# Kernel optimization log

Measured on AMD Instinct MI355X. Metric: run time of the kernel, lower is better.

The kernel has to match this reference:

```python
import jax, jax.numpy as jnp
import numpy as np

DEPTH, HEADS, DIM_HEAD = 3, 8, 64
DIM = 512
MAX_SEQ = 2048
INNER = HEADS * DIM_HEAD  # 512
FF_HID = 4 * DIM          # 2048
EPS = 1e-5


def sparsemax(z):
    # z: (..., n); sparsemax projection onto the simplex (Martins & Astudillo 2016)
    n = z.shape[-1]
    z_sorted = jnp.flip(jnp.sort(z, axis=-1), axis=-1)            # descending
    cs = jnp.cumsum(z_sorted, axis=-1)
    ks = jnp.arange(1, n + 1, dtype=z.dtype)
    support = 1.0 + ks * z_sorted > cs                            # bool
    k_z = jnp.sum(support, axis=-1, keepdims=True)                # int support size
    cs_k = jnp.take_along_axis(cs, k_z - 1, axis=-1)
    tau = (cs_k - 1.0) / k_z.astype(z.dtype)
    return jnp.maximum(z - tau, 0.0)


def layernorm(x, g, b):
    mu = jnp.mean(x, axis=-1, keepdims=True)
    var = jnp.mean(jnp.square(x - mu), axis=-1, keepdims=True)
    return (x - mu) * jax.lax.rsqrt(var + EPS) * g + b


def setup_inputs() -> dict:
    key = jax.random.key(0)
    ks = jax.random.split(key, 12)
    s = 0.02
    inp = {
        "x": jax.random.normal(ks[0], (8, 1024, DIM), dtype=jnp.float32),
        "proj_w": jax.random.normal(ks[1], (DIM, DIM), dtype=jnp.float32) * s,
        "proj_b": jnp.zeros((DIM,), dtype=jnp.float32),
        "pos_emb": jax.random.normal(ks[2], (MAX_SEQ, DIM), dtype=jnp.float32) * s,
        "ln1_g": jnp.ones((DEPTH, DIM), dtype=jnp.float32),
        "ln1_b": jnp.zeros((DEPTH, DIM), dtype=jnp.float32),
        "wqkv": jax.random.normal(ks[3], (DEPTH, DIM, 3 * INNER), dtype=jnp.float32) * s,
        "wout": jax.random.normal(ks[4], (DEPTH, INNER, DIM), dtype=jnp.float32) * s,
        "bout": jnp.zeros((DEPTH, DIM), dtype=jnp.float32),
        "ln2_g": jnp.ones((DEPTH, DIM), dtype=jnp.float32),
        "ln2_b": jnp.zeros((DEPTH, DIM), dtype=jnp.float32),
        "w1": jax.random.normal(ks[5], (DEPTH, DIM, 2 * FF_HID), dtype=jnp.float32) * s,
        "b1": jnp.zeros((DEPTH, 2 * FF_HID), dtype=jnp.float32),
        "w2": jax.random.normal(ks[6], (DEPTH, FF_HID, DIM), dtype=jnp.float32) * s,
        "b2": jnp.zeros((DEPTH, DIM), dtype=jnp.float32),
    }
    return inp


def reference(x, proj_w, proj_b, pos_emb, ln1_g, ln1_b, wqkv, wout, bout,
              ln2_g, ln2_b, w1, b1, w2, b2):
    B, S, D = x.shape
    scale = DIM_HEAD ** -0.5
    x = x @ proj_w + proj_b                       # projection
    x = x + pos_emb[:S][None, :, :]               # positional embedding
    for l in range(DEPTH):
        # --- attention block (Residual(PreNorm(Attention))) ---
        h = layernorm(x, ln1_g[l], ln1_b[l])
        qkv = h @ wqkv[l]                         # (B,S,3*INNER)
        q, k, v = jnp.split(qkv, 3, axis=-1)
        rs = lambda t: t.reshape(B, S, HEADS, DIM_HEAD).transpose(0, 2, 1, 3)
        q, k, v = rs(q), rs(k), rs(v)             # (B,H,S,Dh)
        sim = jnp.einsum('bhid,bhjd->bhij', q, k) * scale
        attn = sparsemax(sim)
        out = jnp.einsum('bhij,bhjd->bhid', attn, v)
        out = out.transpose(0, 2, 1, 3).reshape(B, S, INNER)
        x = x + (out @ wout[l] + bout[l])
        # --- feedforward block (Residual(PreNorm(GEGLU FFN))) ---
        h = layernorm(x, ln2_g[l], ln2_b[l])
        hh = h @ w1[l] + b1[l]                    # (B,S,2*FF_HID)
        a, g = jnp.split(hh, 2, axis=-1)
        ff = (a * jax.nn.gelu(g, approximate=False)) @ w2[l] + b2[l]
        x = x + ff
    return jnp.mean(x, axis=1)                    # (B, D) mean pool
```

## Files before the change

### kernel.cpp

```cpp
#include <hip/hip_runtime.h>
#include <stdint.h>

typedef unsigned short u16;
typedef __attribute__((ext_vector_type(8))) short short8;
typedef __attribute__((ext_vector_type(4))) float f32x4;

__device__ __forceinline__ float bf2f(u16 u){
  union { unsigned u; float f; } v; v.u = ((unsigned)u) << 16; return v.f;
}
__device__ __forceinline__ u16 f2bf(float f){
  union { float f; unsigned u; } v; v.f = f;
  unsigned u = v.u;
  return (u16)((u + 0x7FFFu + ((u >> 16) & 1u)) >> 16);
}
__device__ __forceinline__ void g2lds16(const u16* g, u16* lds){
  __builtin_amdgcn_global_load_lds(
      (const __attribute__((address_space(1))) unsigned int*)g,
      (__attribute__((address_space(3))) unsigned int*)lds, 16, 0, 0);
}
__device__ __forceinline__ float gelu_fast(float g){
  float u2 = g * (1.5957691216057308f + 0.0713548162726f * g * g);
  return g * __builtin_amdgcn_rcpf(1.0f + __expf(-u2));
}

__global__ void k_flag(const unsigned* __restrict__ ln1g, int* __restrict__ flag){
  if (threadIdx.x == 0 && blockIdx.x == 0)
    *flag = (ln1g[0] == 0x3F800000u) ? 0 : 1;
}

__global__ void k_cvt_f32(const void* __restrict__ src, float* __restrict__ dst, int n,
                          const int* __restrict__ flag){
  int i = blockIdx.x * blockDim.x + threadIdx.x;
  if (i < n) dst[i] = (*flag) ? bf2f(((const u16*)src)[i]) : ((const float*)src)[i];
}
__global__ void k_cvt_bf16(const void* __restrict__ src, u16* __restrict__ dst, int n,
                           const int* __restrict__ flag){
  int i = blockIdx.x * blockDim.x + threadIdx.x;
  if (i < n) dst[i] = (*flag) ? ((const u16*)src)[i] : f2bf(((const float*)src)[i]);
}

__global__ void k_transpose(const void* __restrict__ src, u16* __restrict__ dst,
                            int K, int N, const int* __restrict__ flag){
  __shared__ u16 tile[32][33];
  int n0 = blockIdx.x * 32, k0 = blockIdx.y * 32;
  size_t zsrc = (size_t)blockIdx.z * K * N;
  size_t zdst = (size_t)blockIdx.z * N * K;
  int tx = threadIdx.x & 31, ty = threadIdx.x >> 5;
  bool isbf = (*flag) != 0;
  const float* sf = (const float*)src; const u16* sb = (const u16*)src;
  #pragma unroll
  for (int p = 0; p < 4; ++p){
    int kk = k0 + p*8 + ty, nn = n0 + tx;
    size_t idx = zsrc + (size_t)kk * N + nn;
    tile[tx][p*8+ty] = isbf ? sb[idx] : f2bf(sf[idx]);
  }
  __syncthreads();
  #pragma unroll
  for (int p = 0; p < 4; ++p){
    int nn = n0 + p*8 + ty, kk = k0 + tx;
    dst[zdst + (size_t)nn * K + kk] = tile[p*8+ty][tx];
  }
}

__global__ __launch_bounds__(256) void k_ln(const float* __restrict__ x,
                                            const float* __restrict__ g,
                                            const float* __restrict__ b,
                                            u16* __restrict__ out){
  int wv = threadIdx.x >> 6, lane = threadIdx.x & 63;
  int row = blockIdx.x * 4 + wv;
  const float* xr = x + (size_t)row * 512 + lane * 8;
  float4 v0 = *(const float4*)xr;
  float4 v1 = *(const float4*)(xr + 4);
  float s  = v0.x+v0.y+v0.z+v0.w + v1.x+v1.y+v1.z+v1.w;
  float ss = v0.x*v0.x+v0.y*v0.y+v0.z*v0.z+v0.w*v0.w
           + v1.x*v1.x+v1.y*v1.y+v1.z*v1.z+v1.w*v1.w;
  #pragma unroll
  for (int off = 1; off < 64; off <<= 1){ s += __shfl_xor(s, off, 64); ss += __shfl_xor(ss, off, 64); }
  float mu = s * (1.f/512.f);
  float var = ss * (1.f/512.f) - mu*mu;
  float rs = rsqrtf(var + 1e-5f);
  const float* gp = g + lane*8; const float* bp = b + lane*8;
  float4 g0 = *(const float4*)gp, g1 = *(const float4*)(gp+4);
  float4 b0 = *(const float4*)bp, b1 = *(const float4*)(bp+4);
  u16 o[8];
  o[0]=f2bf((v0.x-mu)*rs*g0.x+b0.x); o[1]=f2bf((v0.y-mu)*rs*g0.y+b0.y);
  o[2]=f2bf((v0.z-mu)*rs*g0.z+b0.z); o[3]=f2bf((v0.w-mu)*rs*g0.w+b0.w);
  o[4]=f2bf((v1.x-mu)*rs*g1.x+b1.x); o[5]=f2bf((v1.y-mu)*rs*g1.y+b1.y);
  o[6]=f2bf((v1.z-mu)*rs*g1.z+b1.z); o[7]=f2bf((v1.w-mu)*rs*g1.w+b1.w);
  *(uint4*)(out + (size_t)row*512 + lane*8) = *(const uint4*)o;
}

__global__ __launch_bounds__(256) void k_gemm(const u16* __restrict__ A,
                                              const u16* __restrict__ Wt, int K, int mode,
                                              float* __restrict__ xres, u16* __restrict__ out16,
                                              const float* __restrict__ bias,
                                              const float* __restrict__ pos){
  __shared__ u16 As[128*64];
  __shared__ u16 Bs[128*64];
  const int tid = threadIdx.x;
  const int wv = tid >> 6, lane = tid & 63;
  const int lm = lane & 15, lq = lane >> 4;
  const int wm = (wv >> 1) * 64, wn = (wv & 1) * 64;
  const int m0 = blockIdx.y * 128, n0 = blockIdx.x * 128;
  const int lrow = lane >> 3;
  const int scol = ((lane & 7) ^ lrow) << 3;
  f32x4 acc[4][4];
  #pragma unroll
  for (int i = 0; i < 4; ++i)
    #pragma unroll
    for (int j = 0; j < 4; ++j){ f32x4 z = {0.f,0.f,0.f,0.f}; acc[i][j] = z; }

  for (int k0 = 0; k0 < K; k0 += 64){
    #pragma unroll
    for (int it = 0; it < 4; ++it){
      int ci = wv*4 + it;
      int row = ci*8 + lrow;
      g2lds16(&A [(size_t)(m0 + row) * K + k0 + scol], &As[ci*512]);
      g2lds16(&Wt[(size_t)(n0 + row) * K + k0 + scol], &Bs[ci*512]);
    }
    __syncthreads();
    #pragma unroll
    for (int kk = 0; kk < 2; ++kk){
      short8 af[4], bf[4];
      #pragma unroll
      for (int t = 0; t < 4; ++t){
        int cs = ((kk*4 + lq) ^ (lm & 7)) << 3;
        af[t] = *(const short8*)&As[(wm + t*16 + lm)*64 + cs];
        bf[t] = *(const short8*)&Bs[(wn + t*16 + lm)*64 + cs];
      }
      #pragma unroll
      for (int i = 0; i < 4; ++i)
        #pragma unroll
        for (int j = 0; j < 4; ++j)
          acc[i][j] = __builtin_amdgcn_mfma_f32_16x16x32_bf16(af[i], bf[j], acc[i][j], 0, 0, 0);
    }
    __syncthreads();
  }
  #pragma unroll
  for (int i = 0; i < 4; ++i)
    #pragma unroll
    for (int j = 0; j < 4; ++j)
      #pragma unroll
      for (int r = 0; r < 4; ++r){
        int row = m0 + wm + i*16 + lq*4 + r;
        int col = n0 + wn + j*16 + lm;
        float v = acc[i][j][r];
        if (mode == 0){
          xres[(size_t)row*512 + col] = v + bias[col] + pos[(size_t)(row & 1023)*512 + col];
        } else if (mode == 1){
          int part = col >> 9, within = col & 511;
          int head = within >> 6, dh = within & 63;
          int b = row >> 10, s = row & 1023;
          int bh = b*8 + head;
          size_t o;
          if (part < 2) o = (size_t)part*4194304 + (((size_t)bh*1024 + s) << 6) + dh;
          else          o = (size_t)8388608 + (size_t)bh*65536 + (size_t)dh*1024 + s;
          out16[o] = f2bf(v);
        } else {
          size_t idx = (size_t)row*512 + col;
          xres[idx] = xres[idx] + v + bias[col];
        }
      }
}

__global__ __launch_bounds__(256) void k_gemm64(const u16* __restrict__ A,
                                                const u16* __restrict__ Wt, int K, int mode,
                                                float* __restrict__ xres,
                                                const float* __restrict__ bias,
                                                const float* __restrict__ pos){
  __shared__ u16 As[64*64];
  __shared__ u16 Bs[128*64];
  const int tid = threadIdx.x;
  const int wv = tid >> 6, lane = tid & 63;
  const int lm = lane & 15, lq = lane >> 4;
  const int wm = (wv >> 1) * 32, wn = (wv & 1) * 64;
  const int m0 = blockIdx.y * 64, n0 = blockIdx.x * 128;
  const int lrow = lane >> 3;
  const int scol = ((lane & 7) ^ lrow) << 3;
  f32x4 acc[2][4];
  #pragma unroll
  for (int i = 0; i < 2; ++i)
    #pragma unroll
    for (int j = 0; j < 4; ++j){ f32x4 z = {0.f,0.f,0.f,0.f}; acc[i][j] = z; }

  for (int k0 = 0; k0 < K; k0 += 64){
    #pragma unroll
    for (int it = 0; it < 2; ++it){
      int ci = wv*2 + it;
      int row = ci*8 + lrow;
      g2lds16(&A[(size_t)(m0 + row) * K + k0 + scol], &As[ci*512]);
    }
    #pragma unroll
    for (int it = 0; it < 4; ++it){
      int ci = wv*4 + it;
      int row = ci*8 + lrow;
      g2lds16(&Wt[(size_t)(n0 + row) * K + k0 + scol], &Bs[ci*512]);
    }
    __syncthreads();
    #pragma unroll
    for (int kk = 0; kk < 2; ++kk){
      short8 af[2], bf[4];
      int cs = ((kk*4 + lq) ^ (lm & 7)) << 3;
      #pragma unroll
      for (int t = 0; t < 2; ++t)
        af[t] = *(const short8*)&As[(wm + t*16 + lm)*64 + cs];
      #pragma unroll
      for (int t = 0; t < 4; ++t)
        bf[t] = *(const short8*)&Bs[(wn + t*16 + lm)*64 + cs];
      #pragma unroll
      for (int i = 0; i < 2; ++i)
        #pragma unroll
        for (int j = 0; j < 4; ++j)
          acc[i][j] = __builtin_amdgcn_mfma_f32_16x16x32_bf16(af[i], bf[j], acc[i][j], 0, 0, 0);
    }
    __syncthreads();
  }
  #pragma unroll
  for (int i = 0; i < 2; ++i)
    #pragma unroll
    for (int j = 0; j < 4; ++j)
      #pragma unroll
      for (int r = 0; r < 4; ++r){
        int row = m0 + wm + i*16 + lq*4 + r;
        int col = n0 + wn + j*16 + lm;
        float v = acc[i][j][r];
        if (mode == 0){
          xres[(size_t)row*512 + col] = v + bias[col] + pos[(size_t)(row & 1023)*512 + col];
        } else {
          size_t idx = (size_t)row*512 + col;
          xres[idx] = xres[idx] + v + bias[col];
        }
      }
}

__global__ __launch_bounds__(256) void k_ff1_geglu64(const u16* __restrict__ A,
                                                     const u16* __restrict__ W1t,
                                                     const float* __restrict__ b1,
                                                     u16* __restrict__ ffh){
  __shared__ u16 As[64*64];
  __shared__ u16 Ba[128*64];
  __shared__ u16 Bg[128*64];
  const int tid = threadIdx.x;
  const int wv = tid >> 6, lane = tid & 63;
  const int lm = lane & 15, lq = lane >> 4;
  const int wm = (wv >> 1) * 32, wn = (wv & 1) * 64;
  const int m0 = blockIdx.y * 64, n0 = blockIdx.x * 128;
  const int lrow = lane >> 3;
  const int scol = ((lane & 7) ^ lrow) << 3;
  const int K = 512;
  f32x4 aa[2][4], ag[2][4];
  #pragma unroll
  for (int i = 0; i < 2; ++i)
    #pragma unroll
    for (int j = 0; j < 4; ++j){ f32x4 z = {0.f,0.f,0.f,0.f}; aa[i][j] = z; ag[i][j] = z; }
  for (int k0 = 0; k0 < K; k0 += 64){
    #pragma unroll
    for (int it = 0; it < 2; ++it){
      int ci = wv*2 + it;
      int row = ci*8 + lrow;
      g2lds16(&A[(size_t)(m0 + row) * K + k0 + scol], &As[ci*512]);
    }
    #pragma unroll
    for (int it = 0; it < 4; ++it){
      int ci = wv*4 + it;
      int row = ci*8 + lrow;
      g2lds16(&W1t[(size_t)(n0 + row) * K + k0 + scol],        &Ba[ci*512]);
      g2lds16(&W1t[(size_t)(2048 + n0 + row) * K + k0 + scol], &Bg[ci*512]);
    }
    __syncthreads();
    #pragma unroll
    for (int kk = 0; kk < 2; ++kk){
      short8 af[2], ba[4], bg[4];
      int cs = ((kk*4 + lq) ^ (lm & 7)) << 3;
      #pragma unroll
      for (int t = 0; t < 2; ++t)
        af[t] = *(const short8*)&As[(wm + t*16 + lm)*64 + cs];
      #pragma unroll
      for (int t = 0; t < 4; ++t){
        ba[t] = *(const short8*)&Ba[(wn + t*16 + lm)*64 + cs];
        bg[t] = *(const short8*)&Bg[(wn + t*16 + lm)*64 + cs];
      }
      #pragma unroll
      for (int i = 0; i < 2; ++i)
        #pragma unroll
        for (int j = 0; j < 4; ++j){
          aa[i][j] = __builtin_amdgcn_mfma_f32_16x16x32_bf16(af[i], ba[j], aa[i][j], 0, 0, 0);
          ag[i][j] = __builtin_amdgcn_mfma_f32_16x16x32_bf16(af[i], bg[j], ag[i][j], 0, 0, 0);
        }
    }
    __syncthreads();
  }
  #pragma unroll
  for (int i = 0; i < 2; ++i)
    #pragma unroll
    for (int j = 0; j < 4; ++j)
      #pragma unroll
      for (int r = 0; r < 4; ++r){
        int row = m0 + wm + i*16 + lq*4 + r;
        int n = n0 + wn + j*16 + lm;
        float a = aa[i][j][r] + b1[n];
        float g = ag[i][j][r] + b1[2048 + n];
        ffh[(size_t)row*2048 + n] = f2bf(a * gelu_fast(g));
      }
}

__global__ __launch_bounds__(256) void k_qk(const u16* __restrict__ qb,
                                            const u16* __restrict__ kb,
                                            u16* __restrict__ S, int bh0){
  __shared__ u16 As[128*64];
  __shared__ u16 Bs[128*64];
  const int tid = threadIdx.x;
  const int wv = tid >> 6, lane = tid & 63;
  const int lm = lane & 15, lq = lane >> 4;
  const int wm = (wv >> 1) * 64, wn = (wv & 1) * 64;
  const int m0 = blockIdx.y * 128, n0 = blockIdx.x * 128;
  const int lrow = lane >> 3;
  const int scol = ((lane & 7) ^ lrow) << 3;
  const size_t base = (size_t)(bh0 + blockIdx.z) * 65536;
  f32x4 acc[4][4];
  #pragma unroll
  for (int i = 0; i < 4; ++i)
    #pragma unroll
    for (int j = 0; j < 4; ++j){ f32x4 z = {0.f,0.f,0.f,0.f}; acc[i][j] = z; }

  #pragma unroll
  for (int it = 0; it < 4; ++it){
    int ci = wv*4 + it;
    int row = ci*8 + lrow;
    g2lds16(&qb[base + (size_t)(m0 + row) * 64 + scol], &As[ci*512]);
    g2lds16(&kb[base + (size_t)(n0 + row) * 64 + scol], &Bs[ci*512]);
  }
  __syncthreads();
  #pragma unroll
  for (int kk = 0; kk < 2; ++kk){
    short8 af[4], bf[4];
    #pragma unroll
    for (int t = 0; t < 4; ++t){
      int cs = ((kk*4 + lq) ^ (lm & 7)) << 3;
      af[t] = *(const short8*)&As[(wm + t*16 + lm)*64 + cs];
      bf[t] = *(const short8*)&Bs[(wn + t*16 + lm)*64 + cs];
    }
    #pragma unroll
    for (int i = 0; i < 4; ++i)
      #pragma unroll
      for (int j = 0; j < 4; ++j)
        acc[i][j] = __builtin_amdgcn_mfma_f32_16x16x32_bf16(af[i], bf[j], acc[i][j], 0, 0, 0);
  }
  size_t sb = (size_t)blockIdx.z * 1048576;
  #pragma unroll
  for (int i = 0; i < 4; ++i)
    #pragma unroll
    for (int j = 0; j < 4; ++j)
      #pragma unroll
      for (int r = 0; r < 4; ++r){
        int row = m0 + wm + i*16 + lq*4 + r;
        int col = n0 + wn + j*16 + lm;
        S[sb + (size_t)row*1024 + col] = f2bf(acc[i][j][r] * 0.125f);
      }
}

__global__ __launch_bounds__(256) void k_spmax(const u16* __restrict__ S,
                                               u16* __restrict__ P){
  const int lane = threadIdx.x & 63;
  const int row = blockIdx.x * 4 + (threadIdx.x >> 6);
  const u16* src = S + (size_t)row * 1024 + lane * 16;
  u16 zb[16];
  *(uint4*)zb       = *(const uint4*)src;
  *(uint4*)(zb + 8) = *(const uint4*)(src + 8);
  float z[16];
  #pragma unroll
  for (int i = 0; i < 16; ++i) z[i] = bf2f(zb[i]);
  float s = 0.f;
  #pragma unroll
  for (int i = 0; i < 16; ++i) s += z[i];
  #pragma unroll
  for (int off = 1; off < 64; off <<= 1) s += __shfl_xor(s, off, 64);
  float tau = (s - 1.0f) * (1.0f/1024.0f);
  int prevc = 1024;
  for (int it = 0; it < 48; ++it){
    float s2 = 0.f; int c = 0;
    #pragma unroll
    for (int i = 0; i < 16; ++i){
      float p = z[i] - tau;
      s2 += (p > 0.f ? p : 0.f);
      c += (int)__popcll(__ballot(z[i] > tau));
    }
    #pragma unroll
    for (int off = 1; off < 64; off <<= 1) s2 += __shfl_xor(s2, off, 64);
    tau += (s2 - 1.0f) / (float)c;
    if (c == prevc) break;
    prevc = c;
  }
  u16 tmp[16];
  #pragma unroll
  for (int i = 0; i < 16; ++i){
    float p = z[i] - tau; p = p > 0.f ? p : 0.f;
    tmp[i] = f2bf(p);
  }
  u16* dst = P + (size_t)row * 1024 + lane * 16;
  *(uint4*)dst       = *(const uint4*)tmp;
  *(uint4*)(dst + 8) = *(const uint4*)(tmp + 8);
}

__global__ __launch_bounds__(256) void k_pv(const u16* __restrict__ P,
                                            const u16* __restrict__ vt,
                                            u16* __restrict__ aout, int bh0){
  __shared__ u16 As[64*64];
  __shared__ u16 Bs[64*64];
  const int tid = threadIdx.x;
  const int wv = tid >> 6, lane = tid & 63;
  const int lm = lane & 15, lq = lane >> 4;
  const int m0 = blockIdx.x * 64;
  const int bh = bh0 + blockIdx.y;
  const size_t pbase = (size_t)blockIdx.y * 1048576;
  const size_t vbase = (size_t)bh * 65536;
  const int lrow = lane >> 3;
  const int scol = ((lane & 7) ^ lrow) << 3;
  f32x4 acc[4];
  #pragma unroll
  for (int j = 0; j < 4; ++j){ f32x4 z = {0.f,0.f,0.f,0.f}; acc[j] = z; }

  for (int k0 = 0; k0 < 1024; k0 += 64){
    #pragma unroll
    for (int it = 0; it < 2; ++it){
      int ci = wv*2 + it;
      int row = ci*8 + lrow;
      g2lds16(&P [pbase + (size_t)(m0 + row) * 1024 + k0 + scol], &As[ci*512]);
      g2lds16(&vt[vbase + (size_t)row * 1024 + k0 + scol],        &Bs[ci*512]);
    }
    __syncthreads();
    #pragma unroll
    for (int kk = 0; kk < 2; ++kk){
      int csa = ((kk*4 + lq) ^ (lm & 7)) << 3;
      short8 af = *(const short8*)&As[(wv*16 + lm)*64 + csa];
      #pragma unroll
      for (int j = 0; j < 4; ++j){
        short8 bf = *(const short8*)&Bs[(j*16 + lm)*64 + csa];
        acc[j] = __builtin_amdgcn_mfma_f32_16x16x32_bf16(af, bf, acc[j], 0, 0, 0);
      }
    }
    __syncthreads();
  }
  int b = bh >> 3, h = bh & 7;
  #pragma unroll
  for (int j = 0; j < 4; ++j)
    #pragma unroll
    for (int r = 0; r < 4; ++r){
      int s = m0 + wv*16 + lq*4 + r;
      int d = j*16 + lm;
      aout[((size_t)(b*1024 + s))*512 + h*64 + d] = f2bf(acc[j][r]);
    }
}

__global__ __launch_bounds__(256) void k_attn(const u16* __restrict__ qb,
                                              const u16* __restrict__ kb,
                                              const u16* __restrict__ vt,
                                              u16* __restrict__ aout){
  extern __shared__ char smem[];
  float* sc = (float*)smem;
  u16*  P   = (u16*)smem;
  u16*  Qs  = (u16*)(smem + 131072);
  u16*  KVs = (u16*)(smem + 131072 + 4608);
  const int tid = threadIdx.x;
  const int wv = tid >> 6, lane = tid & 63;
  const int lm = lane & 15, lq = lane >> 4;
  const int bh = blockIdx.y, s0 = blockIdx.x * 32;
  const size_t base = (size_t)bh * 65536;
  {
    int r = tid >> 3, c = tid & 7;
    *(uint4*)&Qs[r*72 + (c << 3)] = *(const uint4*)&qb[base + (size_t)(s0 + r)*64 + (c << 3)];
  }
  for (int kt = 0; kt < 16; ++kt){
    __syncthreads();
    #pragma unroll
    for (int it = 0; it < 2; ++it){
      int s = it*256 + tid; int r = s >> 3, c = s & 7;
      *(uint4*)&KVs[r*72 + (c << 3)] =
          *(const uint4*)&kb[base + (size_t)(kt*64 + r)*64 + (c << 3)];
    }
    __syncthreads();
    f32x4 accs[2];
    { f32x4 z = {0.f,0.f,0.f,0.f}; accs[0] = z; accs[1] = z; }
    #pragma unroll
    for (int kk = 0; kk < 2; ++kk){
      short8 bfk = *(const short8*)&KVs[(wv*16 + lm)*72 + kk*32 + lq*8];
      #pragma unroll
      for (int mt = 0; mt < 2; ++mt){
        short8 af = *(const short8*)&Qs[(mt*16 + lm)*72 + kk*32 + lq*8];
        accs[mt] = __builtin_amdgcn_mfma_f32_16x16x32_bf16(af, bfk, accs[mt], 0, 0, 0);
      }
    }
    #pragma unroll
    for (int mt = 0; mt < 2; ++mt)
      #pragma unroll
      for (int r = 0; r < 4; ++r){
        int row = mt*16 + lq*4 + r;
        int col = kt*64 + wv*16 + lm;
        sc[row*1024 + (((col >> 2) ^ (row & 7)) << 2) + (col & 3)] = accs[mt][r] * 0.125f;
      }
  }
  __syncthreads();
  for (int rr = 0; rr < 8; ++rr){
    int row = wv*8 + rr;
    float z[16];
    #pragma unroll
    for (int i = 0; i < 16; ++i){
      int col = lane + (i << 6);
      z[i] = sc[row*1024 + (((col >> 2) ^ (row & 7)) << 2) + (col & 3)];
    }
    bool act[16];
    #pragma unroll
    for (int i = 0; i < 16; ++i) act[i] = true;
    float prevc = -1.f, tau = 0.f;
    for (int it = 0; it < 64; ++it){
      float s = 0.f, c = 0.f;
      #pragma unroll
      for (int i = 0; i < 16; ++i) if (act[i]){ s += z[i]; c += 1.f; }
      #pragma unroll
      for (int off = 1; off < 64; off <<= 1){ s += __shfl_xor(s, off, 64); c += __shfl_xor(c, off, 64); }
      tau = (s - 1.0f) / c;
      if (c == prevc) break;
      prevc = c;
      #pragma unroll
      for (int i = 0; i < 16; ++i) act[i] = z[i] > tau;
    }
    #pragma unroll
    for (int i = 0; i < 16; ++i){
      int col = lane + (i << 6);
      float p = z[i] - tau; p = p > 0.f ? p : 0.f;
      P[row*2048 + (((col >> 3) ^ (row & 7)) << 3) + (col & 7)] = f2bf(p);
    }
  }
  f32x4 acco[2];
  { f32x4 z = {0.f,0.f,0.f,0.f}; acco[0] = z; acco[1] = z; }
  for (int kt = 0; kt < 16; ++kt){
    __syncthreads();
    {
      int dc = tid >> 6, key = tid & 63;
      #pragma unroll
      for (int j = 0; j < 16; ++j)
        KVs[(dc*16 + j)*72 + key] = vt[base + (size_t)(dc*16 + j)*1024 + kt*64 + key];
    }
    __syncthreads();
    #pragma unroll
    for (int kk = 0; kk < 2; ++kk){
      short8 bfv = *(const short8*)&KVs[(wv*16 + lm)*72 + kk*32 + lq*8];
      #pragma unroll
      for (int mt = 0; mt < 2; ++mt){
        int m = mt*16 + lm;
        int k = kt*64 + kk*32 + lq*8;
        short8 af = *(const short8*)&P[m*2048 + (((k >> 3) ^ (m & 7)) << 3)];
        acco[mt] = __builtin_amdgcn_mfma_f32_16x16x32_bf16(af, bfv, acco[mt], 0, 0, 0);
      }
    }
  }
  int b = bh >> 3, h = bh & 7;
  #pragma unroll
  for (int mt = 0; mt < 2; ++mt)
    #pragma unroll
    for (int r = 0; r < 4; ++r){
      int row = mt*16 + lq*4 + r;
      int s = s0 + row;
      aout[((size_t)(b*1024 + s))*512 + h*64 + wv*16 + lm] = f2bf(acco[mt][r]);
    }
}

__global__ __launch_bounds__(256) void k_pool1(const float* __restrict__ xres,
                                               float* __restrict__ part){
  int b = blockIdx.y, ch = blockIdx.x, tid = threadIdx.x;
  float a0 = 0.f, a1 = 0.f;
  for (int i = 0; i < 64; ++i){
    const float* r = xres + ((size_t)(b*1024 + ch*64 + i)) * 512;
    a0 += r[tid]; a1 += r[tid + 256];
  }
  part[((size_t)(b*16 + ch))*512 + tid]       = a0;
  part[((size_t)(b*16 + ch))*512 + tid + 256] = a1;
}
__global__ __launch_bounds__(512) void k_pool2(const float* __restrict__ part,
                                               void* __restrict__ out,
                                               const int* __restrict__ flag){
  int b = blockIdx.x, d = threadIdx.x;
  float s = 0.f;
  for (int c = 0; c < 16; ++c) s += part[((size_t)(b*16 + c))*512 + d];
  s *= (1.0f/1024.0f);
  if (*flag) ((u16*)out)[b*512 + d] = f2bf(s);
  else       ((float*)out)[b*512 + d] = s;
}

extern "C" void kernel_launch(void* const* d_in, const int* in_sizes, int n_in,
                              void* d_out, int out_size, void* d_ws, size_t ws_size,
                              hipStream_t stream){
  (void)in_sizes; (void)n_in; (void)out_size;
  char* w = (char*)d_ws;
  size_t off = 0;
  auto alloc = [&](size_t bytes) -> char* {
    char* p = w + off;
    off += (bytes + 255) & ~(size_t)255;
    return p;
  };
  int*   flag  = (int*)  alloc(4);
  float* xres  = (float*)alloc((size_t)8192*512*4);
  u16*   hb    = (u16*)  alloc((size_t)8192*512*2);
  u16*   qb    = (u16*)  alloc((size_t)8388608);
  u16*   kb    = (u16*)  alloc((size_t)8388608);
  u16*   vtb   = (u16*)  alloc((size_t)8388608);
  u16*   aoutb = (u16*)  alloc((size_t)8388608);
  u16*   ffh   = qb;
  u16*   pwT   = (u16*)  alloc((size_t)512*512*2);
  u16*   wqkvT = (u16*)  alloc((size_t)3*1536*512*2);
  u16*   woutT = (u16*)  alloc((size_t)3*512*512*2);
  u16*   w1T   = (u16*)  alloc((size_t)3*4096*512*2);
  u16*   w2T   = (u16*)  alloc((size_t)3*512*2048*2);
  float* posf  = (float*)alloc((size_t)1024*512*4);
  float* pbf   = (float*)alloc(512*4);
  float* ln1gf = (float*)alloc(1536*4);
  float* ln1bf = (float*)alloc(1536*4);
  float* ln2gf = (float*)alloc(1536*4);
  float* ln2bf = (float*)alloc(1536*4);
  float* boutf = (float*)alloc(1536*4);
  float* b1f   = (float*)alloc(12288*4);
  float* b2f   = (float*)alloc(1536*4);
  float* part  = (float*)alloc((size_t)8*16*512*4);

  int chunk = 0;
  u16* Sbuf = nullptr; u16* Pbuf = nullptr;
  {
    size_t rem = (ws_size > off) ? (ws_size - off) : 0;
    for (int c = 64; c >= 8; c >>= 1){
      size_t need = (size_t)c * 1048576 * 4 + 512;
      if (need <= rem){
        Sbuf = (u16*)alloc((size_t)c * 1048576 * 2);
        Pbuf = (u16*)alloc((size_t)c * 1048576 * 2);
        chunk = c;
        break;
      }
    }
  }

  const void* x_raw = d_in[0];  const void* projw = d_in[1];  const void* projb = d_in[2];
  const void* pose  = d_in[3];  const void* ln1g  = d_in[4];  const void* ln1b  = d_in[5];
  const void* wqkv  = d_in[6];  const void* wout  = d_in[7];  const void* bout  = d_in[8];
  const void* ln2g  = d_in[9];  const void* ln2b  = d_in[10]; const void* w1    = d_in[11];
  const void* b1    = d_in[12]; const void* w2    = d_in[13]; const void* b2    = d_in[14];

  k_flag<<<1, 1, 0, stream>>>((const unsigned*)ln1g, flag);

  k_transpose<<<dim3(16, 16, 1), 256, 0, stream>>>(projw, pwT,   512,  512, flag);
  k_transpose<<<dim3(48, 16, 3), 256, 0, stream>>>(wqkv,  wqkvT, 512, 1536, flag);
  k_transpose<<<dim3(16, 16, 3), 256, 0, stream>>>(wout,  woutT, 512,  512, flag);
  k_transpose<<<dim3(128,16, 3), 256, 0, stream>>>(w1,    w1T,   512, 4096, flag);
  k_transpose<<<dim3(16, 64, 3), 256, 0, stream>>>(w2,    w2T,  2048,  512, flag);

  k_cvt_f32<<<2,    256, 0, stream>>>(projb, pbf,    512,    flag);
  k_cvt_f32<<<2048, 256, 0, stream>>>(pose,  posf,   524288, flag);
  k_cvt_f32<<<6,    256, 0, stream>>>(ln1g,  ln1gf,  1536,   flag);
  k_cvt_f32<<<6,    256, 0, stream>>>(ln1b,  ln1bf,  1536,   flag);
  k_cvt_f32<<<6,    256, 0, stream>>>(ln2g,  ln2gf,  1536,   flag);
  k_cvt_f32<<<6,    256, 0, stream>>>(ln2b,  ln2bf,  1536,   flag);
  k_cvt_f32<<<6,    256, 0, stream>>>(bout,  boutf,  1536,   flag);
  k_cvt_f32<<<48,   256, 0, stream>>>(b1,    b1f,    12288,  flag);
  k_cvt_f32<<<6,    256, 0, stream>>>(b2,    b2f,    1536,   flag);
  k_cvt_bf16<<<16384, 256, 0, stream>>>(x_raw, hb, 4194304, flag);

  k_gemm64<<<dim3(4, 128), 256, 0, stream>>>(hb, pwT, 512, 0, xres, pbf, posf);

  for (int l = 0; l < 3; ++l){
    k_ln<<<2048, 256, 0, stream>>>(xres, ln1gf + l*512, ln1bf + l*512, hb);
    k_gemm<<<dim3(12, 64), 256, 0, stream>>>(hb, wqkvT + (size_t)l*1536*512, 512, 1,
                                             nullptr, qb, nullptr, nullptr);
    if (chunk){
      for (int bh0 = 0; bh0 < 64; bh0 += chunk){
        k_qk<<<dim3(8, 8, chunk), 256, 0, stream>>>(qb, kb, Sbuf, bh0);
        k_spmax<<<chunk*256, 256, 0, stream>>>(Sbuf, Pbuf);
        k_pv<<<dim3(16, chunk), 256, 0, stream>>>(Pbuf, vtb, aoutb, bh0);
      }
    } else {
      k_attn<<<dim3(32, 64), 256, 144896, stream>>>(qb, kb, vtb, aoutb);
    }
    k_gemm64<<<dim3(4, 128), 256, 0, stream>>>(aoutb, woutT + (size_t)l*512*512, 512, 2,
                                               xres, boutf + l*512, nullptr);
    k_ln<<<2048, 256, 0, stream>>>(xres, ln2gf + l*512, ln2bf + l*512, hb);
    k_ff1_geglu64<<<dim3(16, 128), 256, 0, stream>>>(hb, w1T + (size_t)l*4096*512,
                                                     b1f + l*4096, ffh);
    k_gemm64<<<dim3(4, 128), 256, 0, stream>>>(ffh, w2T + (size_t)l*512*2048, 2048, 2,
                                               xres, b2f + l*512, nullptr);
  }
  k_pool1<<<dim3(16, 8), 256, 0, stream>>>(xres, part);
  k_pool2<<<8, 512, 0, stream>>>(part, d_out, flag);
}
```

Measured before the change: 1.080 ms.

## Fuse QK, sparsemax and PV into one LDS-resident attention kernel

Replaces the three-kernel attention path (QK scores to global, sparsemax, PV) and the old fallback with a single kernel. Each 256-thread block handles 16 query rows of one head, keeps the 16x1024 bf16 score tile in swizzled LDS, runs sparsemax in place, then does PV straight from LDS. A block-id remap spreads heads across the grid. This removes the large global score and probability round trips and most launches, but each block rereads K and V from global without LDS staging, and the sparsemax iteration now starts from the minimum threshold, which may need more iterations.

```diff
diff --git a/kernel.cpp b/kernel.cpp
--- a/kernel.cpp
+++ b/kernel.cpp
@@ -304,265 +304,90 @@
       }
 }
 
-__global__ __launch_bounds__(256) void k_qk(const u16* __restrict__ qb,
-                                            const u16* __restrict__ kb,
-                                            u16* __restrict__ S, int bh0){
-  __shared__ u16 As[128*64];
-  __shared__ u16 Bs[128*64];
+__global__ __launch_bounds__(256) void k_attn2(const u16* __restrict__ qb,
+                                               const u16* __restrict__ kb,
+                                               const u16* __restrict__ vt,
+                                               u16* __restrict__ aout){
+  __shared__ u16 Sm[16*1024];
   const int tid = threadIdx.x;
   const int wv = tid >> 6, lane = tid & 63;
   const int lm = lane & 15, lq = lane >> 4;
-  const int wm = (wv >> 1) * 64, wn = (wv & 1) * 64;
-  const int m0 = blockIdx.y * 128, n0 = blockIdx.x * 128;
-  const int lrow = lane >> 3;
-  const int scol = ((lane & 7) ^ lrow) << 3;
-  const size_t base = (size_t)(bh0 + blockIdx.z) * 65536;
-  f32x4 acc[4][4];
-  #pragma unroll
-  for (int i = 0; i < 4; ++i)
-    #pragma unroll
-    for (int j = 0; j < 4; ++j){ f32x4 z = {0.f,0.f,0.f,0.f}; acc[i][j] = z; }
-
-  #pragma unroll
-  for (int it = 0; it < 4; ++it){
-    int ci = wv*4 + it;
-    int row = ci*8 + lrow;
-    g2lds16(&qb[base + (size_t)(m0 + row) * 64 + scol], &As[ci*512]);
-    g2lds16(&kb[base + (size_t)(n0 + row) * 64 + scol], &Bs[ci*512]);
+  int fid = blockIdx.x;
+  int nf = (fid & 7) * 512 + (fid >> 3);
+  const int bh = nf >> 6;
+  const int q0 = (nf & 63) * 16;
+  const size_t base = (size_t)bh * 65536;
+  const u16* qp = &qb[base + (size_t)(q0 + lm)*64 + lq*8];
+  short8 qf0 = *(const short8*)qp;
+  short8 qf1 = *(const short8*)(qp + 32);
+  for (int kt = 0; kt < 16; ++kt){
+    const u16* kp = &kb[base + (size_t)(kt*64 + wv*16 + lm)*64 + lq*8];
+    short8 kf0 = *(const short8*)kp;
+    short8 kf1 = *(const short8*)(kp + 32);
+    f32x4 a = {0.f,0.f,0.f,0.f};
+    a = __builtin_amdgcn_mfma_f32_16x16x32_bf16(qf0, kf0, a, 0, 0, 0);
+    a = __builtin_amdgcn_mfma_f32_16x16x32_bf16(qf1, kf1, a, 0, 0, 0);
+    int col = kt*64 + wv*16 + lm;
+    int cc = col >> 3, c7 = col & 7;
+    #pragma unroll
+    for (int r = 0; r < 4; ++r){
+      int row = lq*4 + r;
+      Sm[row*1024 + ((cc ^ (row & 7)) << 3) + c7] = f2bf(a[r] * 0.125f);
+    }
   }
   __syncthreads();
-  #pragma unroll
-  for (int kk = 0; kk < 2; ++kk){
-    short8 af[4], bf[4];
-    #pragma unroll
-    for (int t = 0; t < 4; ++t){
-      int cs = ((kk*4 + lq) ^ (lm & 7)) << 3;
-      af[t] = *(const short8*)&As[(wm + t*16 + lm)*64 + cs];
-      bf[t] = *(const short8*)&Bs[(wn + t*16 + lm)*64 + cs];
-    }
-    #pragma unroll
-    for (int i = 0; i < 4; ++i)
-      #pragma unroll
-      for (int j = 0; j < 4; ++j)
-        acc[i][j] = __builtin_amdgcn_mfma_f32_16x16x32_bf16(af[i], bf[j], acc[i][j], 0, 0, 0);
-  }
-  size_t sb = (size_t)blockIdx.z * 1048576;
-  #pragma unroll
-  for (int i = 0; i < 4; ++i)
-    #pragma unroll
-    for (int j = 0; j < 4; ++j)
-      #pragma unroll
-      for (int r = 0; r < 4; ++r){
-        int row = m0 + wm + i*16 + lq*4 + r;
-        int col = n0 + wn + j*16 + lm;
-        S[sb + (size_t)row*1024 + col] = f2bf(acc[i][j][r] * 0.125f);
-      }
-}
-
-__global__ __launch_bounds__(256) void k_spmax(const u16* __restrict__ S,
-                                               u16* __restrict__ P){
-  const int lane = threadIdx.x & 63;
-  const int row = blockIdx.x * 4 + (threadIdx.x >> 6);
-  const u16* src = S + (size_t)row * 1024 + lane * 16;
-  u16 zb[16];
-  *(uint4*)zb       = *(const uint4*)src;
-  *(uint4*)(zb + 8) = *(const uint4*)(src + 8);
-  float z[16];
-  #pragma unroll
-  for (int i = 0; i < 16; ++i) z[i] = bf2f(zb[i]);
-  float s = 0.f;
-  #pragma unroll
-  for (int i = 0; i < 16; ++i) s += z[i];
-  #pragma unroll
-  for (int off = 1; off < 64; off <<= 1) s += __shfl_xor(s, off, 64);
-  float tau = (s - 1.0f) * (1.0f/1024.0f);
-  int prevc = 1024;
-  for (int it = 0; it < 48; ++it){
-    float s2 = 0.f; int c = 0;
+  #pragma unroll 1
+  for (int rr = 0; rr < 4; ++rr){
+    int row = wv*4 + rr;
+    int r7 = row & 7;
+    u16* lo = &Sm[row*1024 + ((lane ^ r7) << 3)];
+    u16* hi = &Sm[row*1024 + (((64 + lane) ^ r7) << 3)];
+    u16 zb[16];
+    *(uint4*)zb       = *(const uint4*)lo;
+    *(uint4*)(zb + 8) = *(const uint4*)hi;
+    float z[16];
+    #pragma unroll
+    for (int i = 0; i < 16; ++i) z[i] = bf2f(zb[i]);
+    float tau = -3.0e38f;
+    int prevc = -1;
+    for (int it = 0; it < 48; ++it){
+      float sz = 0.f; int c = 0;
+      #pragma unroll
+      for (int i = 0; i < 16; ++i){
+        bool aq = z[i] > tau;
+        sz += aq ? z[i] : 0.f;
+        c  += (int)__popcll(__ballot(aq));
+      }
+      #pragma unroll
+      for (int off = 1; off < 64; off <<= 1) sz += __shfl_xor(sz, off, 64);
+      tau = (sz - 1.0f) / (float)c;
+      if (c == prevc) break;
+      prevc = c;
+    }
+    u16 pb[16];
     #pragma unroll
     for (int i = 0; i < 16; ++i){
       float p = z[i] - tau;
-      s2 += (p > 0.f ? p : 0.f);
-      c += (int)__popcll(__ballot(z[i] > tau));
-    }
-    #pragma unroll
-    for (int off = 1; off < 64; off <<= 1) s2 += __shfl_xor(s2, off, 64);
-    tau += (s2 - 1.0f) / (float)c;
-    if (c == prevc) break;
-    prevc = c;
-  }
-  u16 tmp[16];
-  #pragma unroll
-  for (int i = 0; i < 16; ++i){
-    float p = z[i] - tau; p = p > 0.f ? p : 0.f;
-    tmp[i] = f2bf(p);
-  }
-  u16* dst = P + (size_t)row * 1024 + lane * 16;
-  *(uint4*)dst       = *(const uint4*)tmp;
-  *(uint4*)(dst + 8) = *(const uint4*)(tmp + 8);
-}
-
-__global__ __launch_bounds__(256) void k_pv(const u16* __restrict__ P,
-                                            const u16* __restrict__ vt,
-                                            u16* __restrict__ aout, int bh0){
-  __shared__ u16 As[64*64];
-  __shared__ u16 Bs[64*64];
-  const int tid = threadIdx.x;
-  const int wv = tid >> 6, lane = tid & 63;
-  const int lm = lane & 15, lq = lane >> 4;
-  const int m0 = blockIdx.x * 64;
-  const int bh = bh0 + blockIdx.y;
-  const size_t pbase = (size_t)blockIdx.y * 1048576;
-  const size_t vbase = (size_t)bh * 65536;
-  const int lrow = lane >> 3;
-  const int scol = ((lane & 7) ^ lrow) << 3;
-  f32x4 acc[4];
-  #pragma unroll
-  for (int j = 0; j < 4; ++j){ f32x4 z = {0.f,0.f,0.f,0.f}; acc[j] = z; }
-
-  for (int k0 = 0; k0 < 1024; k0 += 64){
-    #pragma unroll
-    for (int it = 0; it < 2; ++it){
-      int ci = wv*2 + it;
-      int row = ci*8 + lrow;
-      g2lds16(&P [pbase + (size_t)(m0 + row) * 1024 + k0 + scol], &As[ci*512]);
-      g2lds16(&vt[vbase + (size_t)row * 1024 + k0 + scol],        &Bs[ci*512]);
-    }
-    __syncthreads();
-    #pragma unroll
-    for (int kk = 0; kk < 2; ++kk){
-      int csa = ((kk*4 + lq) ^ (lm & 7)) << 3;
-      short8 af = *(const short8*)&As[(wv*16 + lm)*64 + csa];
-      #pragma unroll
-      for (int j = 0; j < 4; ++j){
-        short8 bf = *(const short8*)&Bs[(j*16 + lm)*64 + csa];
-        acc[j] = __builtin_amdgcn_mfma_f32_16x16x32_bf16(af, bf, acc[j], 0, 0, 0);
-      }
-    }
-    __syncthreads();
+      pb[i] = f2bf(p > 0.f ? p : 0.f);
+    }
+    *(uint4*)lo = *(const uint4*)pb;
+    *(uint4*)hi = *(const uint4*)(pb + 8);
+  }
+  __syncthreads();
+  f32x4 acc = {0.f,0.f,0.f,0.f};
+  const u16* vrow = &vt[base + (size_t)(wv*16 + lm)*1024 + lq*8];
+  for (int k0 = 0; k0 < 1024; k0 += 32){
+    int cc = (k0 >> 3) + lq;
+    short8 pa = *(const short8*)&Sm[lm*1024 + ((cc ^ (lm & 7)) << 3)];
+    short8 vb = *(const short8*)(vrow + k0);
+    acc = __builtin_amdgcn_mfma_f32_16x16x32_bf16(pa, vb, acc, 0, 0, 0);
   }
   int b = bh >> 3, h = bh & 7;
   #pragma unroll
-  for (int j = 0; j < 4; ++j)
-    #pragma unroll
-    for (int r = 0; r < 4; ++r){
-      int s = m0 + wv*16 + lq*4 + r;
-      int d = j*16 + lm;
-      aout[((size_t)(b*1024 + s))*512 + h*64 + d] = f2bf(acc[j][r]);
-    }
-}
-
-__global__ __launch_bounds__(256) void k_attn(const u16* __restrict__ qb,
-                                              const u16* __restrict__ kb,
-                                              const u16* __restrict__ vt,
-                                              u16* __restrict__ aout){
-  extern __shared__ char smem[];
-  float* sc = (float*)smem;
-  u16*  P   = (u16*)smem;
-  u16*  Qs  = (u16*)(smem + 131072);
-  u16*  KVs = (u16*)(smem + 131072 + 4608);
-  const int tid = threadIdx.x;
-  const int wv = tid >> 6, lane = tid & 63;
-  const int lm = lane & 15, lq = lane >> 4;
-  const int bh = blockIdx.y, s0 = blockIdx.x * 32;
-  const size_t base = (size_t)bh * 65536;
-  {
-    int r = tid >> 3, c = tid & 7;
-    *(uint4*)&Qs[r*72 + (c << 3)] = *(const uint4*)&qb[base + (size_t)(s0 + r)*64 + (c << 3)];
-  }
-  for (int kt = 0; kt < 16; ++kt){
-    __syncthreads();
-    #pragma unroll
-    for (int it = 0; it < 2; ++it){
-      int s = it*256 + tid; int r = s >> 3, c = s & 7;
-      *(uint4*)&KVs[r*72 + (c << 3)] =
-          *(const uint4*)&kb[base + (size_t)(kt*64 + r)*64 + (c << 3)];
-    }
-    __syncthreads();
-    f32x4 accs[2];
-    { f32x4 z = {0.f,0.f,0.f,0.f}; accs[0] = z; accs[1] = z; }
-    #pragma unroll
-    for (int kk = 0; kk < 2; ++kk){
-      short8 bfk = *(const short8*)&KVs[(wv*16 + lm)*72 + kk*32 + lq*8];
-      #pragma unroll
-      for (int mt = 0; mt < 2; ++mt){
-        short8 af = *(const short8*)&Qs[(mt*16 + lm)*72 + kk*32 + lq*8];
-        accs[mt] = __builtin_amdgcn_mfma_f32_16x16x32_bf16(af, bfk, accs[mt], 0, 0, 0);
-      }
-    }
-    #pragma unroll
-    for (int mt = 0; mt < 2; ++mt)
-      #pragma unroll
-      for (int r = 0; r < 4; ++r){
-        int row = mt*16 + lq*4 + r;
-        int col = kt*64 + wv*16 + lm;
-        sc[row*1024 + (((col >> 2) ^ (row & 7)) << 2) + (col & 3)] = accs[mt][r] * 0.125f;
-      }
-  }
-  __syncthreads();
-  for (int rr = 0; rr < 8; ++rr){
-    int row = wv*8 + rr;
-    float z[16];
-    #pragma unroll
-    for (int i = 0; i < 16; ++i){
-      int col = lane + (i << 6);
-      z[i] = sc[row*1024 + (((col >> 2) ^ (row & 7)) << 2) + (col & 3)];
-    }
-    bool act[16];
-    #pragma unroll
-    for (int i = 0; i < 16; ++i) act[i] = true;
-    float prevc = -1.f, tau = 0.f;
-    for (int it = 0; it < 64; ++it){
-      float s = 0.f, c = 0.f;
-      #pragma unroll
-      for (int i = 0; i < 16; ++i) if (act[i]){ s += z[i]; c += 1.f; }
-      #pragma unroll
-      for (int off = 1; off < 64; off <<= 1){ s += __shfl_xor(s, off, 64); c += __shfl_xor(c, off, 64); }
-      tau = (s - 1.0f) / c;
-      if (c == prevc) break;
-      prevc = c;
-      #pragma unroll
-      for (int i = 0; i < 16; ++i) act[i] = z[i] > tau;
-    }
-    #pragma unroll
-    for (int i = 0; i < 16; ++i){
-      int col = lane + (i << 6);
-      float p = z[i] - tau; p = p > 0.f ? p : 0.f;
-      P[row*2048 + (((col >> 3) ^ (row & 7)) << 3) + (col & 7)] = f2bf(p);
-    }
-  }
-  f32x4 acco[2];
-  { f32x4 z = {0.f,0.f,0.f,0.f}; acco[0] = z; acco[1] = z; }
-  for (int kt = 0; kt < 16; ++kt){
-    __syncthreads();
-    {
-      int dc = tid >> 6, key = tid & 63;
-      #pragma unroll
-      for (int j = 0; j < 16; ++j)
-        KVs[(dc*16 + j)*72 + key] = vt[base + (size_t)(dc*16 + j)*1024 + kt*64 + key];
-    }
-    __syncthreads();
-    #pragma unroll
-    for (int kk = 0; kk < 2; ++kk){
-      short8 bfv = *(const short8*)&KVs[(wv*16 + lm)*72 + kk*32 + lq*8];
-      #pragma unroll
-      for (int mt = 0; mt < 2; ++mt){
-        int m = mt*16 + lm;
-        int k = kt*64 + kk*32 + lq*8;
-        short8 af = *(const short8*)&P[m*2048 + (((k >> 3) ^ (m & 7)) << 3)];
-        acco[mt] = __builtin_amdgcn_mfma_f32_16x16x32_bf16(af, bfv, acco[mt], 0, 0, 0);
-      }
-    }
-  }
-  int b = bh >> 3, h = bh & 7;
-  #pragma unroll
-  for (int mt = 0; mt < 2; ++mt)
-    #pragma unroll
-    for (int r = 0; r < 4; ++r){
-      int row = mt*16 + lq*4 + r;
-      int s = s0 + row;
-      aout[((size_t)(b*1024 + s))*512 + h*64 + wv*16 + lm] = f2bf(acco[mt][r]);
-    }
+  for (int r = 0; r < 4; ++r){
+    int s = q0 + lq*4 + r;
+    aout[((size_t)(b*1024 + s))*512 + h*64 + wv*16 + lm] = f2bf(acc[r]);
+  }
 }
 
 __global__ __launch_bounds__(256) void k_pool1(const float* __restrict__ xres,
@@ -590,7 +415,7 @@
 extern "C" void kernel_launch(void* const* d_in, const int* in_sizes, int n_in,
                               void* d_out, int out_size, void* d_ws, size_t ws_size,
                               hipStream_t stream){
-  (void)in_sizes; (void)n_in; (void)out_size;
+  (void)in_sizes; (void)n_in; (void)out_size; (void)ws_size;
   char* w = (char*)d_ws;
   size_t off = 0;
   auto alloc = [&](size_t bytes) -> char* {
@@ -622,21 +447,6 @@
   float* b2f   = (float*)alloc(1536*4);
   float* part  = (float*)alloc((size_t)8*16*512*4);
 
-  int chunk = 0;
-  u16* Sbuf = nullptr; u16* Pbuf = nullptr;
-  {
-    size_t rem = (ws_size > off) ? (ws_size - off) : 0;
-    for (int c = 64; c >= 8; c >>= 1){
-      size_t need = (size_t)c * 1048576 * 4 + 512;
-      if (need <= rem){
-        Sbuf = (u16*)alloc((size_t)c * 1048576 * 2);
-        Pbuf = (u16*)alloc((size_t)c * 1048576 * 2);
-        chunk = c;
-        break;
-      }
-    }
-  }
-
   const void* x_raw = d_in[0];  const void* projw = d_in[1];  const void* projb = d_in[2];
   const void* pose  = d_in[3];  const void* ln1g  = d_in[4];  const void* ln1b  = d_in[5];
   const void* wqkv  = d_in[6];  const void* wout  = d_in[7];  const void* bout  = d_in[8];
@@ -668,15 +478,7 @@
     k_ln<<<2048, 256, 0, stream>>>(xres, ln1gf + l*512, ln1bf + l*512, hb);
     k_gemm<<<dim3(12, 64), 256, 0, stream>>>(hb, wqkvT + (size_t)l*1536*512, 512, 1,
                                              nullptr, qb, nullptr, nullptr);
-    if (chunk){
-      for (int bh0 = 0; bh0 < 64; bh0 += chunk){
-        k_qk<<<dim3(8, 8, chunk), 256, 0, stream>>>(qb, kb, Sbuf, bh0);
-        k_spmax<<<chunk*256, 256, 0, stream>>>(Sbuf, Pbuf);
-        k_pv<<<dim3(16, chunk), 256, 0, stream>>>(Pbuf, vtb, aoutb, bh0);
-      }
-    } else {
-      k_attn<<<dim3(32, 64), 256, 144896, stream>>>(qb, kb, vtb, aoutb);
-    }
+    k_attn2<<<dim3(4096), 256, 0, stream>>>(qb, kb, vtb, aoutb);
     k_gemm64<<<dim3(4, 128), 256, 0, stream>>>(aoutb, woutT + (size_t)l*512*512, 512, 2,
                                                xres, boutf + l*512, nullptr);
     k_ln<<<2048, 256, 0, stream>>>(xres, ln2gf + l*512, ln2bf + l*512, hb);
```

Result: faster. 1.054 ms (-2.4%).
